# Optimization experiments

Measured on AMD Instinct MI355X. Metric: run time of the kernel, lower is better.

The kernel has to match this reference:

```python
import jax, jax.numpy as jnp
import numpy as np

B, G, FI, FO, H, W = 16, 8, 64, 64, 64, 64
N_ITER = 3


def setup_inputs() -> dict:
    key = jax.random.key(0)
    kx, kw, kb = jax.random.split(key, 3)
    x = jax.random.normal(kx, (B, G * FI, H, W), dtype=jnp.float32)
    # kaiming_normal_ on [fo*g, fi, 1, 1]: std = sqrt(2 / fan_in), fan_in = fi*1*1
    weight = jax.random.normal(kw, (FO * G, FI, 1, 1), dtype=jnp.float32) * np.sqrt(2.0 / FI)
    bias = jax.random.normal(kb, (1, FO, 1, 1), dtype=jnp.float32) * 0.01
    return {"x": x, "weight": weight, "bias": bias}


def reference(x, weight, bias):
    g, n_iter = G, N_ITER
    gfo, fi = weight.shape[:2]
    fo = gfo // g
    b, c, h, w = x.shape
    # grouped 1x1 conv == per-group channel matmul
    xg = x.reshape(b, g, fi, h, w)
    wg = weight.reshape(g, fo, fi)
    con = jnp.einsum('bgihw,gfi->bgfhw', xg, wg)  # [B, g, fo, H, W]
    beta = jnp.zeros((), dtype=x.dtype)
    for i in range(n_iter):
        alpha = jax.nn.sigmoid(beta)
        v = jnp.sum(alpha * con, axis=1, keepdims=True)  # [B, 1, fo, H, W]
        if i == n_iter - 1:
            out = v[:, 0]  # [B, fo, H, W]
            return out + bias
        beta = beta + jnp.sum(v * con, axis=2, keepdims=True)  # [B, g, 1, H, W]
```

## Files before the change

kernel.cpp:

```cpp
#include <hip/hip_runtime.h>


typedef __attribute__((ext_vector_type(8))) _Float16 half8;
typedef __attribute__((ext_vector_type(4))) float f32x4;

#define NG   8
#define NFI  64
#define NFO  64
#define HW   4096

__device__ __forceinline__ float sigmoidf_fast(float v) {
    float e = __builtin_amdgcn_exp2f(-1.44269504088896f * v);
    return __builtin_amdgcn_rcpf(1.0f + e);
}

__global__ __launch_bounds__(256)
void wconv_kernel(const float* __restrict__ w, _Float16* __restrict__ wbuf) {
    int V = blockIdx.x * 256 + threadIdx.x;
    int g    = V >> 10;
    int t    = (V >> 8) & 3;
    int c    = (V >> 6) & 3;
    int lane = V & 63;
    int pl = lane & 15, q = lane >> 4;
    const float* src = w + g * (NFO * NFI) + (t * 16 + pl) * NFI + (c & 1) * 32 + q * 8;
    half8 o;
    #pragma unroll
    for (int j = 0; j < 8; ++j) {
        float f = src[j];
        _Float16 h = (_Float16)f;
        o[j] = (c >> 1) ? (_Float16)(f - (float)h) : h;
    }
    *(half8*)(wbuf + (size_t)V * 8) = o;
}

__global__ __launch_bounds__(256, 2)
void routing_kernel(const float* __restrict__ x,
                    const _Float16* __restrict__ wbuf,
                    const float* __restrict__ bias,
                    float* __restrict__ out) {
    const int tid  = threadIdx.x;
    const int b    = blockIdx.x >> 6;
    const int p0   = (blockIdx.x & 63) << 6;
    const int lane = tid & 63;
    const int wv   = tid >> 6;
    const int pl   = lane & 15;
    const int q    = lane >> 4;
    const int pw   = wv * 16 + pl;

    __shared__ _Float16 wlds[2][16 * 512];

    const float* xg = x + (size_t)b * (NG * NFI) * HW + p0 + pw;

    f32x4 acc[NG][4];
    #pragma unroll
    for (int g = 0; g < NG; ++g)
        #pragma unroll
        for (int t = 0; t < 4; ++t)
            acc[g][t] = (f32x4){0.f, 0.f, 0.f, 0.f};

#define CB   asm volatile("" ::: "memory")
#define BAR  __builtin_amdgcn_s_barrier()
#define SB0  __builtin_amdgcn_sched_barrier(0)
#define WAITV(N) asm volatile("s_waitcnt vmcnt(" #N ")" ::: "memory")

#define WSTAGE(G, BUF)                                                        \
    {                                                                         \
        const _Float16* ws_ = wbuf + (size_t)(G) * 8192 + (wv * 4) * 512 + lane * 8; \
        _Float16* wd_ = &wlds[BUF][0] + (wv * 4) * 512;                       \
        __builtin_amdgcn_global_load_lds(                                     \
            (const __attribute__((address_space(1))) void*)(ws_),             \
            (__attribute__((address_space(3))) void*)(wd_), 16, 0, 0);        \
        __builtin_amdgcn_global_load_lds(                                     \
            (const __attribute__((address_space(1))) void*)(ws_ + 512),       \
            (__attribute__((address_space(3))) void*)(wd_ + 512), 16, 0, 0);  \
        __builtin_amdgcn_global_load_lds(                                     \
            (const __attribute__((address_space(1))) void*)(ws_ + 1024),      \
            (__attribute__((address_space(3))) void*)(wd_ + 1024), 16, 0, 0); \
        __builtin_amdgcn_global_load_lds(                                     \
            (const __attribute__((address_space(1))) void*)(ws_ + 1536),      \
            (__attribute__((address_space(3))) void*)(wd_ + 1536), 16, 0, 0); \
    }

#define XDECL(NM) float NM##0, NM##1, NM##2, NM##3, NM##4, NM##5, NM##6, NM##7, \
                        NM##8, NM##9, NM##10, NM##11, NM##12, NM##13, NM##14, NM##15;
#define XLOAD(G, NM)                                                         \
    {                                                                        \
        const float* p_ = xg + (size_t)((G) * 64 + q * 8) * HW;              \
        NM##0 = p_[(size_t)0 * HW];  NM##1 = p_[(size_t)1 * HW];             \
        NM##2 = p_[(size_t)2 * HW];  NM##3 = p_[(size_t)3 * HW];             \
        NM##4 = p_[(size_t)4 * HW];  NM##5 = p_[(size_t)5 * HW];             \
        NM##6 = p_[(size_t)6 * HW];  NM##7 = p_[(size_t)7 * HW];             \
        const float* p2_ = p_ + (size_t)32 * HW;                             \
        NM##8  = p2_[(size_t)0 * HW]; NM##9  = p2_[(size_t)1 * HW];          \
        NM##10 = p2_[(size_t)2 * HW]; NM##11 = p2_[(size_t)3 * HW];          \
        NM##12 = p2_[(size_t)4 * HW]; NM##13 = p2_[(size_t)5 * HW];          \
        NM##14 = p2_[(size_t)6 * HW]; NM##15 = p2_[(size_t)7 * HW];          \
    }
#define XGRP(G, NM, BUF)                                                     \
    {                                                                        \
        half8 b0, b1;                                                        \
        b0[0] = (_Float16)NM##0;  b0[1] = (_Float16)NM##1;                   \
        b0[2] = (_Float16)NM##2;  b0[3] = (_Float16)NM##3;                   \
        b0[4] = (_Float16)NM##4;  b0[5] = (_Float16)NM##5;                   \
        b0[6] = (_Float16)NM##6;  b0[7] = (_Float16)NM##7;                   \
        b1[0] = (_Float16)NM##8;  b1[1] = (_Float16)NM##9;                   \
        b1[2] = (_Float16)NM##10; b1[3] = (_Float16)NM##11;                  \
        b1[4] = (_Float16)NM##12; b1[5] = (_Float16)NM##13;                  \
        b1[6] = (_Float16)NM##14; b1[7] = (_Float16)NM##15;                  \
        const _Float16* wg_ = &wlds[BUF][0] + lane * 8;                      \
        _Pragma("unroll")                                                    \
        for (int t = 0; t < 4; ++t) {                                        \
            const _Float16* wp_ = wg_ + (size_t)t * 2048;                    \
            half8 a0h = *(const half8*)(wp_);                                \
            half8 a1h = *(const half8*)(wp_ + 512);                          \
            half8 a0l = *(const half8*)(wp_ + 1024);                         \
            half8 a1l = *(const half8*)(wp_ + 1536);                         \
            acc[G][t] = __builtin_amdgcn_mfma_f32_16x16x32_f16(a0h, b0, acc[G][t], 0, 0, 0); \
            acc[G][t] = __builtin_amdgcn_mfma_f32_16x16x32_f16(a1h, b1, acc[G][t], 0, 0, 0); \
            acc[G][t] = __builtin_amdgcn_mfma_f32_16x16x32_f16(a0l, b0, acc[G][t], 0, 0, 0); \
            acc[G][t] = __builtin_amdgcn_mfma_f32_16x16x32_f16(a1l, b1, acc[G][t], 0, 0, 0); \
        }                                                                    \
    }

    XDECL(X0) XDECL(X1) XDECL(X2)

    WSTAGE(0, 0); CB;
    XLOAD(0, X0); CB;
    WSTAGE(1, 1); CB;
    XLOAD(1, X1); CB;

    XLOAD(2, X2); WAITV(36); BAR; SB0; XGRP(0, X0, 0); BAR; WSTAGE(2, 0); CB;
    XLOAD(3, X0); WAITV(36); BAR; SB0; XGRP(1, X1, 1); BAR; WSTAGE(3, 1); CB;
    XLOAD(4, X1); WAITV(36); BAR; SB0; XGRP(2, X2, 0); BAR; WSTAGE(4, 0); CB;
    XLOAD(5, X2); WAITV(36); BAR; SB0; XGRP(3, X0, 1); BAR; WSTAGE(5, 1); CB;
    XLOAD(6, X0); WAITV(36); BAR; SB0; XGRP(4, X1, 0); BAR; WSTAGE(6, 0); CB;
    XLOAD(7, X1); WAITV(36); BAR; SB0; XGRP(5, X2, 1); BAR; WSTAGE(7, 1); CB;
                  WAITV(20); BAR; SB0; XGRP(6, X0, 0);
                  WAITV(0);  BAR; SB0; XGRP(7, X1, 1);

#undef XDECL
#undef XLOAD
#undef XGRP
#undef WSTAGE
#undef CB
#undef BAR
#undef SB0
#undef WAITV

    float v0[4][4];
    #pragma unroll
    for (int t = 0; t < 4; ++t)
        #pragma unroll
        for (int r = 0; r < 4; ++r) {
            float s = 0.f;
            #pragma unroll
            for (int g = 0; g < NG; ++g) s += acc[g][t][r];
            v0[t][r] = 0.5f * s;
        }

    float beta[NG], alpha[NG];
    #pragma unroll
    for (int g = 0; g < NG; ++g) {
        float s = 0.f;
        #pragma unroll
        for (int t = 0; t < 4; ++t)
            #pragma unroll
            for (int r = 0; r < 4; ++r)
                s += v0[t][r] * acc[g][t][r];
        s += __shfl_xor(s, 16);
        s += __shfl_xor(s, 32);
        beta[g]  = s;
        alpha[g] = sigmoidf_fast(s);
    }

    #pragma unroll
    for (int t = 0; t < 4; ++t)
        #pragma unroll
        for (int r = 0; r < 4; ++r) {
            float s = 0.f;
            #pragma unroll
            for (int g = 0; g < NG; ++g) s += alpha[g] * acc[g][t][r];
            v0[t][r] = s;
        }
    #pragma unroll
    for (int g = 0; g < NG; ++g) {
        float s = 0.f;
        #pragma unroll
        for (int t = 0; t < 4; ++t)
            #pragma unroll
            for (int r = 0; r < 4; ++r)
                s += v0[t][r] * acc[g][t][r];
        s += __shfl_xor(s, 16);
        s += __shfl_xor(s, 32);
        beta[g] += s;
        alpha[g] = sigmoidf_fast(beta[g]);
    }

    #pragma unroll
    for (int t = 0; t < 4; ++t)
        #pragma unroll
        for (int r = 0; r < 4; ++r) {
            int f = t * 16 + q * 4 + r;
            float s = bias[f];
            #pragma unroll
            for (int g = 0; g < NG; ++g) s += alpha[g] * acc[g][t][r];
            out[((size_t)(b * NFO + f)) * HW + p0 + pw] = s;
        }
}

extern "C" void kernel_launch(void* const* d_in, const int* in_sizes, int n_in,
                              void* d_out, int out_size, void* d_ws, size_t ws_size,
                              hipStream_t stream) {
    const float* x    = (const float*)d_in[0];
    const float* w    = (const float*)d_in[1];
    const float* bias = (const float*)d_in[2];
    float* out = (float*)d_out;
    _Float16* wbuf = (_Float16*)d_ws;

    wconv_kernel<<<32, 256, 0, stream>>>(w, wbuf);
    routing_kernel<<<1024, 256, 0, stream>>>(x, wbuf, bias, out);
}
```

Before: 206.2 us.

## Stage x tiles into LDS via async global_load_lds with swizzled layout

Replaces the per-thread scalar global loads of x into registers with 16-byte global_load_lds transfers into a double-buffered LDS tile, alongside the weight staging. The x tile is written with an XOR-like rotation and read back per lane with matching offsets, then converted to fp16 for the MFMAs. The goal is wider, coalesced loads and fewer VGPRs held for in-flight x data. In exchange it adds 32 KB of LDS per block and LDS read traffic, which may limit occupancy at two blocks per CU, and the pipeline depth drops from three register sets in flight to two LDS buffers.

```diff
diff --git a/kernel.cpp b/kernel.cpp
--- a/kernel.cpp
+++ b/kernel.cpp
@@ -47,9 +47,19 @@
     const int q    = lane >> 4;
     const int pw   = wv * 16 + pl;
 
+    __shared__ float    xlds[2][64 * 64];
     __shared__ _Float16 wlds[2][16 * 512];
 
-    const float* xg = x + (size_t)b * (NG * NFI) * HW + p0 + pw;
+    const float* xbase = x + (size_t)b * (NG * NFI) * HW;
+
+#define MKXS(c) \
+    const int   ch##c = wv * 16 + (c) * 4 + q; \
+    const float* xs##c = xbase + (size_t)ch##c * HW + p0 + ((pl * 4 - 8 * (ch##c >> 3)) & 63);
+    MKXS(0) MKXS(1) MKXS(2) MKXS(3)
+#undef MKXS
+
+    const int rb0 = q * 512 + ((pw + 8 * q) & 63);
+    const int rb1 = 2048 + q * 512 + ((pw + 8 * q + 32) & 63);
 
     f32x4 acc[NG][4];
     #pragma unroll
@@ -81,32 +91,37 @@
             (__attribute__((address_space(3))) void*)(wd_ + 1536), 16, 0, 0); \
     }
 
-#define XDECL(NM) float NM##0, NM##1, NM##2, NM##3, NM##4, NM##5, NM##6, NM##7, \
-                        NM##8, NM##9, NM##10, NM##11, NM##12, NM##13, NM##14, NM##15;
-#define XLOAD(G, NM)                                                         \
+#define XSTAGE(G, BUF)                                                        \
+    {                                                                         \
+        const size_t go_ = (size_t)(G) * 64 * HW;                             \
+        float* xd_ = &xlds[BUF][0] + (wv * 16) * 64;                          \
+        __builtin_amdgcn_global_load_lds(                                     \
+            (const __attribute__((address_space(1))) void*)(xs0 + go_),       \
+            (__attribute__((address_space(3))) void*)(xd_), 16, 0, 0);        \
+        __builtin_amdgcn_global_load_lds(                                     \
+            (const __attribute__((address_space(1))) void*)(xs1 + go_),       \
+            (__attribute__((address_space(3))) void*)(xd_ + 256), 16, 0, 0);  \
+        __builtin_amdgcn_global_load_lds(                                     \
+            (const __attribute__((address_space(1))) void*)(xs2 + go_),       \
+            (__attribute__((address_space(3))) void*)(xd_ + 512), 16, 0, 0);  \
+        __builtin_amdgcn_global_load_lds(                                     \
+            (const __attribute__((address_space(1))) void*)(xs3 + go_),       \
+            (__attribute__((address_space(3))) void*)(xd_ + 768), 16, 0, 0);  \
+    }
+
+#define XGRP(G, BUF)                                                         \
     {                                                                        \
-        const float* p_ = xg + (size_t)((G) * 64 + q * 8) * HW;              \
-        NM##0 = p_[(size_t)0 * HW];  NM##1 = p_[(size_t)1 * HW];             \
-        NM##2 = p_[(size_t)2 * HW];  NM##3 = p_[(size_t)3 * HW];             \
-        NM##4 = p_[(size_t)4 * HW];  NM##5 = p_[(size_t)5 * HW];             \
-        NM##6 = p_[(size_t)6 * HW];  NM##7 = p_[(size_t)7 * HW];             \
-        const float* p2_ = p_ + (size_t)32 * HW;                             \
-        NM##8  = p2_[(size_t)0 * HW]; NM##9  = p2_[(size_t)1 * HW];          \
-        NM##10 = p2_[(size_t)2 * HW]; NM##11 = p2_[(size_t)3 * HW];          \
-        NM##12 = p2_[(size_t)4 * HW]; NM##13 = p2_[(size_t)5 * HW];          \
-        NM##14 = p2_[(size_t)6 * HW]; NM##15 = p2_[(size_t)7 * HW];          \
-    }
-#define XGRP(G, NM, BUF)                                                     \
-    {                                                                        \
+        const float* xr0_ = &xlds[BUF][0] + rb0;                             \
+        const float* xr1_ = &xlds[BUF][0] + rb1;                             \
         half8 b0, b1;                                                        \
-        b0[0] = (_Float16)NM##0;  b0[1] = (_Float16)NM##1;                   \
-        b0[2] = (_Float16)NM##2;  b0[3] = (_Float16)NM##3;                   \
-        b0[4] = (_Float16)NM##4;  b0[5] = (_Float16)NM##5;                   \
-        b0[6] = (_Float16)NM##6;  b0[7] = (_Float16)NM##7;                   \
-        b1[0] = (_Float16)NM##8;  b1[1] = (_Float16)NM##9;                   \
-        b1[2] = (_Float16)NM##10; b1[3] = (_Float16)NM##11;                  \
-        b1[4] = (_Float16)NM##12; b1[5] = (_Float16)NM##13;                  \
-        b1[6] = (_Float16)NM##14; b1[7] = (_Float16)NM##15;                  \
+        b0[0] = (_Float16)xr0_[0 * 64]; b0[1] = (_Float16)xr0_[1 * 64];      \
+        b0[2] = (_Float16)xr0_[2 * 64]; b0[3] = (_Float16)xr0_[3 * 64];      \
+        b0[4] = (_Float16)xr0_[4 * 64]; b0[5] = (_Float16)xr0_[5 * 64];      \
+        b0[6] = (_Float16)xr0_[6 * 64]; b0[7] = (_Float16)xr0_[7 * 64];      \
+        b1[0] = (_Float16)xr1_[0 * 64]; b1[1] = (_Float16)xr1_[1 * 64];      \
+        b1[2] = (_Float16)xr1_[2 * 64]; b1[3] = (_Float16)xr1_[3 * 64];      \
+        b1[4] = (_Float16)xr1_[4 * 64]; b1[5] = (_Float16)xr1_[5 * 64];      \
+        b1[6] = (_Float16)xr1_[6 * 64]; b1[7] = (_Float16)xr1_[7 * 64];      \
         const _Float16* wg_ = &wlds[BUF][0] + lane * 8;                      \
         _Pragma("unroll")                                                    \
         for (int t = 0; t < 4; ++t) {                                        \
@@ -122,25 +137,20 @@
         }                                                                    \
     }
 
-    XDECL(X0) XDECL(X1) XDECL(X2)
-
-    WSTAGE(0, 0); CB;
-    XLOAD(0, X0); CB;
-    WSTAGE(1, 1); CB;
-    XLOAD(1, X1); CB;
-
-    XLOAD(2, X2); WAITV(36); BAR; SB0; XGRP(0, X0, 0); BAR; WSTAGE(2, 0); CB;
-    XLOAD(3, X0); WAITV(36); BAR; SB0; XGRP(1, X1, 1); BAR; WSTAGE(3, 1); CB;
-    XLOAD(4, X1); WAITV(36); BAR; SB0; XGRP(2, X2, 0); BAR; WSTAGE(4, 0); CB;
-    XLOAD(5, X2); WAITV(36); BAR; SB0; XGRP(3, X0, 1); BAR; WSTAGE(5, 1); CB;
-    XLOAD(6, X0); WAITV(36); BAR; SB0; XGRP(4, X1, 0); BAR; WSTAGE(6, 0); CB;
-    XLOAD(7, X1); WAITV(36); BAR; SB0; XGRP(5, X2, 1); BAR; WSTAGE(7, 1); CB;
-                  WAITV(20); BAR; SB0; XGRP(6, X0, 0);
-                  WAITV(0);  BAR; SB0; XGRP(7, X1, 1);
-
-#undef XDECL
-#undef XLOAD
+    WSTAGE(0, 0); XSTAGE(0, 0); CB;
+    WSTAGE(1, 1); XSTAGE(1, 1); CB;
+
+    WAITV(8); BAR; SB0; XGRP(0, 0); BAR; WSTAGE(2, 0); XSTAGE(2, 0); CB;
+    WAITV(8); BAR; SB0; XGRP(1, 1); BAR; WSTAGE(3, 1); XSTAGE(3, 1); CB;
+    WAITV(8); BAR; SB0; XGRP(2, 0); BAR; WSTAGE(4, 0); XSTAGE(4, 0); CB;
+    WAITV(8); BAR; SB0; XGRP(3, 1); BAR; WSTAGE(5, 1); XSTAGE(5, 1); CB;
+    WAITV(8); BAR; SB0; XGRP(4, 0); BAR; WSTAGE(6, 0); XSTAGE(6, 0); CB;
+    WAITV(8); BAR; SB0; XGRP(5, 1); BAR; WSTAGE(7, 1); XSTAGE(7, 1); CB;
+    WAITV(8); BAR; SB0; XGRP(6, 0); BAR;
+    WAITV(0); BAR; SB0; XGRP(7, 1);
+
 #undef XGRP
+#undef XSTAGE
 #undef WSTAGE
 #undef CB
 #undef BAR
```

Measured after the change: 201.4 us. -2.4%, faster.
